# Optimization experiments

Hardware: AMD Instinct MI355X
Metric: run time of the kernel (lower is better)

The kernel has to match this reference:

```python
import jax, jax.numpy as jnp
import numpy as np

jax.config.update("jax_enable_x64", True)

B, S = 256, 256
TINY = float(np.finfo(np.float64).tiny)  # torch.finfo().tiny for double


def _matrix_tree_logZ(scores, mask):
    """scores: [B,S,S] float64, mask: [B,S] bool (col 0 is False).
    Returns sum over batch of log partition function (Matrix-Tree theorem)."""
    lens = mask.sum(-1)  # token counts per sentence (excludes root col)
    mask_r = mask.at[:, 0].set(True)  # index_fill(1, 0, 1)
    pair = mask_r[:, :, None] & mask_r[:, None, :]  # [B,S,S]
    s = jnp.where(pair, scores, -jnp.inf)
    m = jnp.max(s.reshape(s.shape[0], -1), axis=-1)  # [B] per-batch max for stability
    A = jnp.maximum(jnp.exp(s - m[:, None, None]), TINY)  # clamp like torch
    idx = jnp.arange(S)
    D = jnp.zeros_like(A).at[:, idx, idx].set(A.sum(-1))  # degree matrix
    eye = jnp.eye(S, dtype=A.dtype)
    # masked_scatter_: rows with mask_r True take (D - A) rows, else identity
    L = jnp.where(mask_r[:, :, None], D - A, eye)
    logZ = jnp.linalg.slogdet(L[:, 1:, 1:])[1] + m * lens
    return logZ.sum()


def setup_inputs() -> dict:
    key = jax.random.key(0)
    k1, k2 = jax.random.split(key)
    scores = jax.random.normal(k1, (B, S, S), dtype=jnp.float32)
    lens = jax.random.randint(k2, (B,), S // 2, S)  # sentence lengths
    pos = jnp.arange(S)
    # col 0 (pseudo root) False, padding beyond length False
    mask = (pos[None, :] >= 1) & (pos[None, :] < lens[:, None])
    return {"scores": scores, "mask": mask}


def reference(scores, mask):
    # mbr=True path: marginals = d logZ / d scores (computed in double like torch)
    s64 = scores.astype(jnp.float64)
    probs = jax.grad(_matrix_tree_logZ)(s64, mask)
    return probs.astype(jnp.float32)
```

## Files before the change

kernel.cpp:

```cpp
#include <hip/hip_runtime.h>
#include <math.h>


#define S 256
#define BB 256

__device__ __forceinline__ int rowmap(int lr, int kb) {
    int rt = lr >> 6;
    int rb = rt + (rt >= kb ? 1 : 0);
    return rb * 64 + (lr & 63);
}

__global__ __launch_bounds__(256) void k_max(const float* __restrict__ sc,
                                             float* __restrict__ partial) {
    int b = blockIdx.y, rg = blockIdx.x;
    const float4* p4 = (const float4*)(sc + (size_t)b * S * S + rg * 8192);
    int tid = threadIdx.x;
    float4 v[8];
    #pragma unroll
    for (int it = 0; it < 8; ++it) v[it] = p4[tid + 256 * it];
    float m = -1e30f;
    #pragma unroll
    for (int it = 0; it < 8; ++it)
        m = fmaxf(m, fmaxf(fmaxf(v[it].x, v[it].y), fmaxf(v[it].z, v[it].w)));
    for (int off = 32; off > 0; off >>= 1) m = fmaxf(m, __shfl_down(m, off));
    __shared__ float sm[4];
    if ((tid & 63) == 0) sm[tid >> 6] = m;
    __syncthreads();
    if (tid == 0) partial[b * 8 + rg] = fmaxf(fmaxf(sm[0], sm[1]), fmaxf(sm[2], sm[3]));
}

__global__ void k_n(const unsigned char* __restrict__ mk, const float* __restrict__ partial,
                    double* __restrict__ mb, int* __restrict__ nb) {
    int b = blockIdx.x, j = threadIdx.x;
    __shared__ int shc[4];

    const unsigned int* mw = (const unsigned int*)mk;
    unsigned int w0 = mw[0], w1 = mw[1];
    int mode = (w0 != 0u) ? 0 : ((w1 != 0u) ? 1 : 2);

    int c;
    if (mode == 0)      c = (mk[(size_t)b * S + j] != 0);
    else if (mode == 1) c = (((const int*)mk)[(size_t)b * S + j] != 0);
    else                c = (((const long long*)mk)[(size_t)b * S + j] != 0LL);

    int lane = j & 63, wid = j >> 6;
    int cs = c;
    for (int off = 32; off > 0; off >>= 1) cs += __shfl_down(cs, off);
    if (lane == 0) shc[wid] = cs;
    __syncthreads();
    if (j == 0) {
        nb[b] = shc[0] + shc[1] + shc[2] + shc[3];
        float mm = partial[b * 8];
        #pragma unroll
        for (int q = 1; q < 8; ++q) mm = fmaxf(mm, partial[b * 8 + q]);
        mb[b] = (double)mm;
    }
}

__global__ __launch_bounds__(256) void k_build(const float* __restrict__ sc,
                                               const double* __restrict__ mb,
                                               const int* __restrict__ nb,
                                               double* __restrict__ Mg) {
    int b = blockIdx.y;
    int wid = threadIdx.x >> 6, lane = threadIdx.x & 63;
    int p = blockIdx.x * 4 + wid;
    int n = nb[b];
    double m = mb[b];
    __shared__ double se[4][260];
    double* Mrow = Mg + ((size_t)b * S + p) * S;
    bool act = (p < n);
    double ssum = 0.0;
    #pragma unroll
    for (int c4 = 0; c4 < 4; ++c4) {
        int j = lane + 64 * c4;
        double ev = 0.0;
        if (act && j <= n)
            ev = (double)expf((float)((double)sc[((size_t)b * S + (p + 1)) * S + j] - m));
        se[wid][j] = ev;
        ssum += ev;
    }
    for (int off = 32; off > 0; off >>= 1) ssum += __shfl_down(ssum, off);
    ssum = __shfl(ssum, 0);
    __syncthreads();
    #pragma unroll
    for (int c4 = 0; c4 < 4; ++c4) {
        int j = lane + 64 * c4;
        double v;
        if (act && j < n) v = ((j == p) ? ssum : 0.0) - se[wid][j + 1];
        else              v = (j == p) ? 1.0 : 0.0;
        Mrow[j] = v;
    }
}

__global__ __launch_bounds__(512) void k_step(double* __restrict__ Mg, int kb) {
    int b = blockIdx.x;
    double* M = Mg + (size_t)b * S * S;
    int tid = threadIdx.x;
    __shared__ double H[64 * 256];
    __shared__ double SCR[3104];

    int i = tid >> 3, g = tid & 7, c0 = g << 3;
    double c[8];
    {
        const double* src = M + (size_t)(kb * 64 + i) * S + kb * 64 + c0;
        #pragma unroll
        for (int m2 = 0; m2 < 4; ++m2) {
            double2 t = *(const double2*)(src + 2 * m2);
            c[2 * m2] = t.x; c[2 * m2 + 1] = t.y;
        }
    }
    double* rbuf = SCR;
    double* cbuf = SCR + 128;
    if (i == 0) {
        #pragma unroll
        for (int u = 0; u < 8; ++u) rbuf[c0 + u] = c[u];
    }
    if (g == 0) cbuf[i] = c[0];
    for (int k = 0; k < 64; ++k) {
        int par = k & 1;
        __syncthreads();
        double pv = rbuf[par * 64 + k];
        double f  = cbuf[par * 64 + i];
        double rk[8];
        #pragma unroll
        for (int m2 = 0; m2 < 4; ++m2) {
            double2 t = *(const double2*)&rbuf[par * 64 + c0 + 2 * m2];
            rk[2 * m2] = t.x; rk[2 * m2 + 1] = t.y;
        }
        double pivinv = 1.0 / pv;
        int kg = k >> 3, ks = k & 7;
        if (i == k) {
            #pragma unroll
            for (int u = 0; u < 8; ++u)
                c[u] = ((g == kg) && (u == ks)) ? pivinv : c[u] * pivinv;
        } else {
            double gm = f * pivinv;
            #pragma unroll
            for (int u = 0; u < 8; ++u)
                c[u] = ((g == kg) && (u == ks)) ? (-gm) : fma(-gm, rk[u], c[u]);
        }
        int k1 = k + 1;
        if (k1 < 64) {
            if (i == k1) {
                #pragma unroll
                for (int u = 0; u < 8; ++u) rbuf[(par ^ 1) * 64 + c0 + u] = c[u];
            }
            if (g == (k1 >> 3)) cbuf[(par ^ 1) * 64 + i] = c[k1 & 7];
        }
    }
    __syncthreads();

    int tx = tid & 31, ty = tid >> 5;
    double* PT = SCR;
    double* Rc = SCR + 512;
    double2 ga[4][3];
    #pragma unroll
    for (int r = 0; r < 4; ++r)
        #pragma unroll
        for (int q = 0; q < 3; ++q) ga[r][q] = double2{0.0, 0.0};

    for (int cs = 0; cs < 8; ++cs) {
        if (g == cs) {
            #pragma unroll
            for (int u = 0; u < 8; ++u) PT[u * 64 + i] = c[u];
        }
        #pragma unroll
        for (int rep = 0; rep < 3; ++rep) {
            int idx = rep * 512 + tid;
            int sL = idx / 192, jj = idx - sL * 192;
            Rc[sL * 192 + jj] = M[(size_t)(kb * 64 + cs * 8 + sL) * S + rowmap(jj, kb)];
        }
        __syncthreads();
        #pragma unroll
        for (int sL = 0; sL < 8; ++sL) {
            double2 p01 = *(const double2*)&PT[sL * 64 + 4 * ty];
            double2 p23 = *(const double2*)&PT[sL * 64 + 4 * ty + 2];
            double2 r0 = *(const double2*)&Rc[sL * 192 + 2 * tx];
            double2 r1 = *(const double2*)&Rc[sL * 192 + 2 * tx + 64];
            double2 r2 = *(const double2*)&Rc[sL * 192 + 2 * tx + 128];
            ga[0][0].x = fma(p01.x, r0.x, ga[0][0].x); ga[0][0].y = fma(p01.x, r0.y, ga[0][0].y);
            ga[0][1].x = fma(p01.x, r1.x, ga[0][1].x); ga[0][1].y = fma(p01.x, r1.y, ga[0][1].y);
            ga[0][2].x = fma(p01.x, r2.x, ga[0][2].x); ga[0][2].y = fma(p01.x, r2.y, ga[0][2].y);
            ga[1][0].x = fma(p01.y, r0.x, ga[1][0].x); ga[1][0].y = fma(p01.y, r0.y, ga[1][0].y);
            ga[1][1].x = fma(p01.y, r1.x, ga[1][1].x); ga[1][1].y = fma(p01.y, r1.y, ga[1][1].y);
            ga[1][2].x = fma(p01.y, r2.x, ga[1][2].x); ga[1][2].y = fma(p01.y, r2.y, ga[1][2].y);
            ga[2][0].x = fma(p23.x, r0.x, ga[2][0].x); ga[2][0].y = fma(p23.x, r0.y, ga[2][0].y);
            ga[2][1].x = fma(p23.x, r1.x, ga[2][1].x); ga[2][1].y = fma(p23.x, r1.y, ga[2][1].y);
            ga[2][2].x = fma(p23.x, r2.x, ga[2][2].x); ga[2][2].y = fma(p23.x, r2.y, ga[2][2].y);
            ga[3][0].x = fma(p23.y, r0.x, ga[3][0].x); ga[3][0].y = fma(p23.y, r0.y, ga[3][0].y);
            ga[3][1].x = fma(p23.y, r1.x, ga[3][1].x); ga[3][1].y = fma(p23.y, r1.y, ga[3][1].y);
            ga[3][2].x = fma(p23.y, r2.x, ga[3][2].x); ga[3][2].y = fma(p23.y, r2.y, ga[3][2].y);
        }
        __syncthreads();
    }
    #pragma unroll
    for (int r = 0; r < 4; ++r)
        #pragma unroll
        for (int q = 0; q < 3; ++q) {
            int col = rowmap(2 * tx + 64 * q, kb);
            *(double2*)&H[(4 * ty + r) * 256 + col] = ga[r][q];
        }
    #pragma unroll
    for (int u = 0; u < 8; ++u) H[i * 256 + kb * 64 + c0 + u] = c[u];
    __syncthreads();

    #pragma unroll
    for (int rep = 0; rep < 16; ++rep) {
        int idx = rep * 512 + tid;
        int row = idx >> 7, col2 = idx & 127;
        *(double2*)&M[(size_t)(kb * 64 + row) * S + 2 * col2] =
            *(const double2*)&H[row * 256 + 2 * col2];
    }

    double* FT = SCR;
    for (int half = 0; half < 2; ++half) {
        double2 acc[6][4];
        #pragma unroll
        for (int q = 0; q < 6; ++q)
            #pragma unroll
            for (int w = 0; w < 4; ++w) acc[q][w] = double2{0.0, 0.0};

        for (int ck = 0; ck < 4; ++ck) {
            __syncthreads();
            #pragma unroll
            for (int rep = 0; rep < 3; ++rep) {
                int idx = rep * 512 + tid;
                int kk = idx & 15, lr = idx >> 4;
                FT[kk * 194 + lr] =
                    M[(size_t)rowmap(half * 96 + lr, kb) * S + kb * 64 + ck * 16 + kk];
            }
            __syncthreads();
            for (int kk = 0; kk < 16; ++kk) {
                int kr = ck * 16 + kk;
                double2 f01 = *(const double2*)&FT[kk * 194 + 6 * ty];
                double2 f23 = *(const double2*)&FT[kk * 194 + 6 * ty + 2];
                double2 f45 = *(const double2*)&FT[kk * 194 + 6 * ty + 4];
                #pragma unroll
                for (int w = 0; w < 4; ++w) {
                    double2 h = *(const double2*)&H[kr * 256 + 2 * tx + 64 * w];
                    acc[0][w].x = fma(f01.x, h.x, acc[0][w].x); acc[0][w].y = fma(f01.x, h.y, acc[0][w].y);
                    acc[1][w].x = fma(f01.y, h.x, acc[1][w].x); acc[1][w].y = fma(f01.y, h.y, acc[1][w].y);
                    acc[2][w].x = fma(f23.x, h.x, acc[2][w].x); acc[2][w].y = fma(f23.x, h.y, acc[2][w].y);
                    acc[3][w].x = fma(f23.y, h.x, acc[3][w].x); acc[3][w].y = fma(f23.y, h.y, acc[3][w].y);
                    acc[4][w].x = fma(f45.x, h.x, acc[4][w].x); acc[4][w].y = fma(f45.x, h.y, acc[4][w].y);
                    acc[5][w].x = fma(f45.y, h.x, acc[5][w].x); acc[5][w].y = fma(f45.y, h.y, acc[5][w].y);
                }
            }
        }
        #pragma unroll
        for (int q = 0; q < 6; ++q) {
            size_t row = (size_t)rowmap(half * 96 + 6 * ty + q, kb) * S;
            #pragma unroll
            for (int w = 0; w < 4; ++w) {
                int j0 = 2 * tx + 64 * w;
                if (w == kb) {
                    *(double2*)&M[row + j0] = double2{-acc[q][w].x, -acc[q][w].y};
                } else {
                    double2 old = *(const double2*)&M[row + j0];
                    *(double2*)&M[row + j0] = double2{old.x - acc[q][w].x, old.y - acc[q][w].y};
                }
            }
        }
    }
}

__global__ __launch_bounds__(256) void k_xt(const double* __restrict__ Mg,
                                            float* __restrict__ outF,
                                            double* __restrict__ Dg) {
    int b = blockIdx.y, t = blockIdx.x;
    int r = t & 3, c = t >> 2;
    const double* M = Mg + (size_t)b * S * S;
    __shared__ float L[64][65];
    int tid = threadIdx.x;
    int cc = tid & 63;
    #pragma unroll
    for (int rep = 0; rep < 16; ++rep) {
        int rr = rep * 4 + (tid >> 6);
        L[rr][cc] = (float)M[(size_t)(64 * r + rr) * S + 64 * c + cc];
    }
    if (r == c && tid < 64)
        Dg[(size_t)b * S + 64 * r + tid] = M[(size_t)(64 * r + tid) * S + 64 * r + tid];
    __syncthreads();
    int pp = tid & 63;
    #pragma unroll
    for (int rep = 0; rep < 16; ++rep) {
        int qq = rep * 4 + (tid >> 6);
        int orow = 64 * c + qq + 1, ocol = 64 * r + pp + 1;
        if (orow < 256 && ocol < 256)
            outF[((size_t)b * S + orow) * S + ocol] = L[pp][qq];
    }
}

__global__ __launch_bounds__(256) void k_epi2(const float* __restrict__ sc,
                                              const double* __restrict__ Dg,
                                              const double* __restrict__ mb,
                                              const int* __restrict__ nb,
                                              float* __restrict__ out) {
    int b = blockIdx.y;
    int idx4 = blockIdx.x * 256 + threadIdx.x;
    int i = idx4 >> 6;
    int jq = idx4 & 63;
    int n = nb[b];
    float m = (float)mb[b];
    size_t base = ((size_t)b * S + i) * S + 4 * jq;
    float4 xf = *(const float4*)(out + base);
    float4 s4 = *(const float4*)(sc + base);
    double dg = (i >= 1) ? Dg[(size_t)b * S + i - 1] : 0.0;
    float xfa[4] = {xf.x, xf.y, xf.z, xf.w};
    float sa[4]  = {s4.x, s4.y, s4.z, s4.w};
    float ra[4];
    #pragma unroll
    for (int comp = 0; comp < 4; ++comp) {
        int j = 4 * jq + comp;
        float v = 0.0f;
        if (i >= 1 && i <= n && j <= n) {
            double A = (double)expf(sa[comp] - m);
            double sub = (j >= 1) ? (double)xfa[comp] : 0.0;
            v = (float)(A * (dg - sub));
        }
        ra[comp] = v;
    }
    *(float4*)(out + base) = float4{ra[0], ra[1], ra[2], ra[3]};
}

extern "C" void kernel_launch(void* const* d_in, const int* in_sizes, int n_in,
                              void* d_out, int out_size, void* d_ws, size_t ws_size,
                              hipStream_t stream) {
    (void)in_sizes; (void)n_in; (void)out_size; (void)ws_size;
    const float* sc = (const float*)d_in[0];
    const unsigned char* mk = (const unsigned char*)d_in[1];
    double* ws = (double*)d_ws;

    double* M  = ws;
    double* mb = M + (size_t)BB * S * S;
    int*    nb = (int*)(mb + BB);
    double* Dg = mb + 2 * BB;
    float*  partial = (float*)Dg;
    float*  out = (float*)d_out;

    k_max<<<dim3(8, BB), 256, 0, stream>>>(sc, partial);
    k_n<<<BB, 256, 0, stream>>>(mk, partial, mb, nb);
    k_build<<<dim3(64, BB), 256, 0, stream>>>(sc, mb, nb, M);
    for (int kb = 0; kb < 4; ++kb)
        k_step<<<BB, 512, 0, stream>>>(M, kb);
    k_xt<<<dim3(16, BB), 256, 0, stream>>>(M, out, Dg);
    k_epi2<<<dim3(64, BB), 256, 0, stream>>>(sc, Dg, mb, nb, out);
}
```

Measured before the change: 570.7 us.

## Split each block-inversion step across two column-half blocks with double-buffered pivot panel

Each batch's in-place block Gauss-Jordan step now runs as two workgroups, each owning one 128-column half of the matrix. This doubles grid parallelism, and the smaller LDS footprint allows more blocks per CU. The current pivot-column panel is kept in a separate double-buffered F array (placed in the output buffer as scratch). That lets both halves read the unmodified panel without racing on M, and the next panel is written out during the trailing update. The cost is duplicated panel factorization in both blocks, extra global writes for the panel, and reliance on the output buffer being large enough to act as scratch before the final kernels overwrite it.

```diff
diff --git a/kernel.cpp b/kernel.cpp
--- a/kernel.cpp
+++ b/kernel.cpp
@@ -61,7 +61,8 @@
 __global__ __launch_bounds__(256) void k_build(const float* __restrict__ sc,
                                                const double* __restrict__ mb,
                                                const int* __restrict__ nb,
-                                               double* __restrict__ Mg) {
+                                               double* __restrict__ Mg,
+                                               double* __restrict__ Fb) {
     int b = blockIdx.y;
     int wid = threadIdx.x >> 6, lane = threadIdx.x & 63;
     int p = blockIdx.x * 4 + wid;
@@ -90,20 +91,27 @@
         if (act && j < n) v = ((j == p) ? ssum : 0.0) - se[wid][j + 1];
         else              v = (j == p) ? 1.0 : 0.0;
         Mrow[j] = v;
-    }
-}
-
-__global__ __launch_bounds__(512) void k_step(double* __restrict__ Mg, int kb) {
-    int b = blockIdx.x;
+        if (c4 == 0)
+            Fb[((size_t)b * S + p) * 64 + j] = v;
+    }
+}
+
+__global__ __launch_bounds__(512, 4) void k_step2(double* __restrict__ Mg,
+                                                  const double* __restrict__ Fcur,
+                                                  double* __restrict__ Fnext, int kb) {
+    int id = blockIdx.x;
+    int q = id & 1, b = id >> 1;
     double* M = Mg + (size_t)b * S * S;
+    const double* F = Fcur + (size_t)b * (S * 64);
+    double* FN = Fnext + (size_t)b * (S * 64);
     int tid = threadIdx.x;
-    __shared__ double H[64 * 256];
-    __shared__ double SCR[3104];
+    __shared__ double H[64 * 128];
+    __shared__ double SCR[1584];
 
     int i = tid >> 3, g = tid & 7, c0 = g << 3;
     double c[8];
     {
-        const double* src = M + (size_t)(kb * 64 + i) * S + kb * 64 + c0;
+        const double* src = F + (size_t)(kb * 64 + i) * 64 + c0;
         #pragma unroll
         for (int m2 = 0; m2 < 4; ++m2) {
             double2 t = *(const double2*)(src + 2 * m2);
@@ -149,118 +157,129 @@
             if (g == (k1 >> 3)) cbuf[(par ^ 1) * 64 + i] = c[k1 & 7];
         }
     }
-    __syncthreads();
-
-    int tx = tid & 31, ty = tid >> 5;
+
+    int ty = tid >> 5, tx = tid & 31;
     double* PT = SCR;
-    double* Rc = SCR + 512;
-    double2 ga[4][3];
-    #pragma unroll
-    for (int r = 0; r < 4; ++r)
-        #pragma unroll
-        for (int q = 0; q < 3; ++q) ga[r][q] = double2{0.0, 0.0};
-
-    for (int cs = 0; cs < 8; ++cs) {
-        if (g == cs) {
+    double* Rc = SCR + 528;
+    double2 ga[4][2];
+    #pragma unroll
+    for (int r = 0; r < 4; ++r) { ga[r][0] = double2{0.0, 0.0}; ga[r][1] = double2{0.0, 0.0}; }
+
+    for (int cs2 = 0; cs2 < 8; ++cs2) {
+        __syncthreads();
+        if (g == cs2) {
             #pragma unroll
-            for (int u = 0; u < 8; ++u) PT[u * 64 + i] = c[u];
-        }
+            for (int u = 0; u < 8; ++u) PT[u * 66 + i] = c[u];
+        }
+        #pragma unroll
+        for (int rep = 0; rep < 2; ++rep) {
+            int idx = rep * 512 + tid;
+            int kL = idx >> 7, jl = idx & 127;
+            Rc[kL * 132 + jl] = M[(size_t)(kb * 64 + cs2 * 8 + kL) * S + 128 * q + jl];
+        }
+        __syncthreads();
+        #pragma unroll
+        for (int kL = 0; kL < 8; ++kL) {
+            double2 pA = *(const double2*)&PT[kL * 66 + 4 * ty];
+            double2 pB = *(const double2*)&PT[kL * 66 + 4 * ty + 2];
+            double2 r0 = *(const double2*)&Rc[kL * 132 + 2 * tx];
+            double2 r1 = *(const double2*)&Rc[kL * 132 + 2 * tx + 64];
+            ga[0][0].x = fma(pA.x, r0.x, ga[0][0].x); ga[0][0].y = fma(pA.x, r0.y, ga[0][0].y);
+            ga[0][1].x = fma(pA.x, r1.x, ga[0][1].x); ga[0][1].y = fma(pA.x, r1.y, ga[0][1].y);
+            ga[1][0].x = fma(pA.y, r0.x, ga[1][0].x); ga[1][0].y = fma(pA.y, r0.y, ga[1][0].y);
+            ga[1][1].x = fma(pA.y, r1.x, ga[1][1].x); ga[1][1].y = fma(pA.y, r1.y, ga[1][1].y);
+            ga[2][0].x = fma(pB.x, r0.x, ga[2][0].x); ga[2][0].y = fma(pB.x, r0.y, ga[2][0].y);
+            ga[2][1].x = fma(pB.x, r1.x, ga[2][1].x); ga[2][1].y = fma(pB.x, r1.y, ga[2][1].y);
+            ga[3][0].x = fma(pB.y, r0.x, ga[3][0].x); ga[3][0].y = fma(pB.y, r0.y, ga[3][0].y);
+            ga[3][1].x = fma(pB.y, r1.x, ga[3][1].x); ga[3][1].y = fma(pB.y, r1.y, ga[3][1].y);
+        }
+    }
+    #pragma unroll
+    for (int r = 0; r < 4; ++r) {
+        int row = 4 * ty + r;
+        *(double2*)&H[row * 128 + 2 * tx]      = ga[r][0];
+        *(double2*)&H[row * 128 + 64 + 2 * tx] = ga[r][1];
+    }
+    int qp = kb >> 1, po = (kb & 1) << 6;
+    __syncthreads();
+    if (q == qp) {
+        #pragma unroll
+        for (int u = 0; u < 8; ++u) H[i * 128 + po + c0 + u] = c[u];
+    }
+    __syncthreads();
+    #pragma unroll
+    for (int rep = 0; rep < 8; ++rep) {
+        int idx = rep * 512 + tid;
+        int row = idx >> 6, cp = idx & 63;
+        *(double2*)&M[(size_t)(kb * 64 + row) * S + 128 * q + 2 * cp] =
+            *(const double2*)&H[row * 128 + 2 * cp];
+    }
+    int kbn = kb + 1, qn = kbn >> 1, pon = (kbn & 1) << 6;
+    if (kb < 3 && q == qn) {
+        #pragma unroll
+        for (int rep = 0; rep < 4; ++rep) {
+            int idx = rep * 512 + tid;
+            int row = idx >> 5, kp = idx & 31;
+            *(double2*)&FN[(size_t)(kb * 64 + row) * 64 + 2 * kp] =
+                *(const double2*)&H[row * 128 + pon + 2 * kp];
+        }
+    }
+
+    int tz = tid >> 4, txx = tid & 15;
+    double* FT = SCR;
+    double2 acc[6][4];
+    #pragma unroll
+    for (int h = 0; h < 6; ++h)
+        #pragma unroll
+        for (int w = 0; w < 4; ++w) acc[h][w] = double2{0.0, 0.0};
+
+    for (int ck = 0; ck < 8; ++ck) {
+        __syncthreads();
         #pragma unroll
         for (int rep = 0; rep < 3; ++rep) {
             int idx = rep * 512 + tid;
-            int sL = idx / 192, jj = idx - sL * 192;
-            Rc[sL * 192 + jj] = M[(size_t)(kb * 64 + cs * 8 + sL) * S + rowmap(jj, kb)];
-        }
-        __syncthreads();
-        #pragma unroll
-        for (int sL = 0; sL < 8; ++sL) {
-            double2 p01 = *(const double2*)&PT[sL * 64 + 4 * ty];
-            double2 p23 = *(const double2*)&PT[sL * 64 + 4 * ty + 2];
-            double2 r0 = *(const double2*)&Rc[sL * 192 + 2 * tx];
-            double2 r1 = *(const double2*)&Rc[sL * 192 + 2 * tx + 64];
-            double2 r2 = *(const double2*)&Rc[sL * 192 + 2 * tx + 128];
-            ga[0][0].x = fma(p01.x, r0.x, ga[0][0].x); ga[0][0].y = fma(p01.x, r0.y, ga[0][0].y);
-            ga[0][1].x = fma(p01.x, r1.x, ga[0][1].x); ga[0][1].y = fma(p01.x, r1.y, ga[0][1].y);
-            ga[0][2].x = fma(p01.x, r2.x, ga[0][2].x); ga[0][2].y = fma(p01.x, r2.y, ga[0][2].y);
-            ga[1][0].x = fma(p01.y, r0.x, ga[1][0].x); ga[1][0].y = fma(p01.y, r0.y, ga[1][0].y);
-            ga[1][1].x = fma(p01.y, r1.x, ga[1][1].x); ga[1][1].y = fma(p01.y, r1.y, ga[1][1].y);
-            ga[1][2].x = fma(p01.y, r2.x, ga[1][2].x); ga[1][2].y = fma(p01.y, r2.y, ga[1][2].y);
-            ga[2][0].x = fma(p23.x, r0.x, ga[2][0].x); ga[2][0].y = fma(p23.x, r0.y, ga[2][0].y);
-            ga[2][1].x = fma(p23.x, r1.x, ga[2][1].x); ga[2][1].y = fma(p23.x, r1.y, ga[2][1].y);
-            ga[2][2].x = fma(p23.x, r2.x, ga[2][2].x); ga[2][2].y = fma(p23.x, r2.y, ga[2][2].y);
-            ga[3][0].x = fma(p23.y, r0.x, ga[3][0].x); ga[3][0].y = fma(p23.y, r0.y, ga[3][0].y);
-            ga[3][1].x = fma(p23.y, r1.x, ga[3][1].x); ga[3][1].y = fma(p23.y, r1.y, ga[3][1].y);
-            ga[3][2].x = fma(p23.y, r2.x, ga[3][2].x); ga[3][2].y = fma(p23.y, r2.y, ga[3][2].y);
-        }
-        __syncthreads();
-    }
-    #pragma unroll
-    for (int r = 0; r < 4; ++r)
-        #pragma unroll
-        for (int q = 0; q < 3; ++q) {
-            int col = rowmap(2 * tx + 64 * q, kb);
-            *(double2*)&H[(4 * ty + r) * 256 + col] = ga[r][q];
-        }
-    #pragma unroll
-    for (int u = 0; u < 8; ++u) H[i * 256 + kb * 64 + c0 + u] = c[u];
-    __syncthreads();
-
-    #pragma unroll
-    for (int rep = 0; rep < 16; ++rep) {
-        int idx = rep * 512 + tid;
-        int row = idx >> 7, col2 = idx & 127;
-        *(double2*)&M[(size_t)(kb * 64 + row) * S + 2 * col2] =
-            *(const double2*)&H[row * 256 + 2 * col2];
-    }
-
-    double* FT = SCR;
-    for (int half = 0; half < 2; ++half) {
-        double2 acc[6][4];
-        #pragma unroll
-        for (int q = 0; q < 6; ++q)
-            #pragma unroll
-            for (int w = 0; w < 4; ++w) acc[q][w] = double2{0.0, 0.0};
-
-        for (int ck = 0; ck < 4; ++ck) {
-            __syncthreads();
-            #pragma unroll
-            for (int rep = 0; rep < 3; ++rep) {
-                int idx = rep * 512 + tid;
-                int kk = idx & 15, lr = idx >> 4;
-                FT[kk * 194 + lr] =
-                    M[(size_t)rowmap(half * 96 + lr, kb) * S + kb * 64 + ck * 16 + kk];
-            }
-            __syncthreads();
-            for (int kk = 0; kk < 16; ++kk) {
-                int kr = ck * 16 + kk;
-                double2 f01 = *(const double2*)&FT[kk * 194 + 6 * ty];
-                double2 f23 = *(const double2*)&FT[kk * 194 + 6 * ty + 2];
-                double2 f45 = *(const double2*)&FT[kk * 194 + 6 * ty + 4];
-                #pragma unroll
-                for (int w = 0; w < 4; ++w) {
-                    double2 h = *(const double2*)&H[kr * 256 + 2 * tx + 64 * w];
-                    acc[0][w].x = fma(f01.x, h.x, acc[0][w].x); acc[0][w].y = fma(f01.x, h.y, acc[0][w].y);
-                    acc[1][w].x = fma(f01.y, h.x, acc[1][w].x); acc[1][w].y = fma(f01.y, h.y, acc[1][w].y);
-                    acc[2][w].x = fma(f23.x, h.x, acc[2][w].x); acc[2][w].y = fma(f23.x, h.y, acc[2][w].y);
-                    acc[3][w].x = fma(f23.y, h.x, acc[3][w].x); acc[3][w].y = fma(f23.y, h.y, acc[3][w].y);
-                    acc[4][w].x = fma(f45.x, h.x, acc[4][w].x); acc[4][w].y = fma(f45.x, h.y, acc[4][w].y);
-                    acc[5][w].x = fma(f45.y, h.x, acc[5][w].x); acc[5][w].y = fma(f45.y, h.y, acc[5][w].y);
-                }
-            }
-        }
-        #pragma unroll
-        for (int q = 0; q < 6; ++q) {
-            size_t row = (size_t)rowmap(half * 96 + 6 * ty + q, kb) * S;
+            int lr = idx >> 3, kk = idx & 7;
+            FT[kk * 194 + lr] = F[(size_t)rowmap(lr, kb) * 64 + ck * 8 + kk];
+        }
+        __syncthreads();
+        #pragma unroll
+        for (int kk = 0; kk < 8; ++kk) {
+            int kr = ck * 8 + kk;
+            double2 fA = *(const double2*)&FT[kk * 194 + 6 * tz];
+            double2 fB = *(const double2*)&FT[kk * 194 + 6 * tz + 2];
+            double2 fC = *(const double2*)&FT[kk * 194 + 6 * tz + 4];
             #pragma unroll
             for (int w = 0; w < 4; ++w) {
-                int j0 = 2 * tx + 64 * w;
-                if (w == kb) {
-                    *(double2*)&M[row + j0] = double2{-acc[q][w].x, -acc[q][w].y};
-                } else {
-                    double2 old = *(const double2*)&M[row + j0];
-                    *(double2*)&M[row + j0] = double2{old.x - acc[q][w].x, old.y - acc[q][w].y};
-                }
+                double2 h2 = *(const double2*)&H[kr * 128 + 2 * txx + 32 * w];
+                acc[0][w].x = fma(fA.x, h2.x, acc[0][w].x); acc[0][w].y = fma(fA.x, h2.y, acc[0][w].y);
+                acc[1][w].x = fma(fA.y, h2.x, acc[1][w].x); acc[1][w].y = fma(fA.y, h2.y, acc[1][w].y);
+                acc[2][w].x = fma(fB.x, h2.x, acc[2][w].x); acc[2][w].y = fma(fB.x, h2.y, acc[2][w].y);
+                acc[3][w].x = fma(fB.y, h2.x, acc[3][w].x); acc[3][w].y = fma(fB.y, h2.y, acc[3][w].y);
+                acc[4][w].x = fma(fC.x, h2.x, acc[4][w].x); acc[4][w].y = fma(fC.x, h2.y, acc[4][w].y);
+                acc[5][w].x = fma(fC.y, h2.x, acc[5][w].x); acc[5][w].y = fma(fC.y, h2.y, acc[5][w].y);
             }
+        }
+    }
+    bool own_piv  = (q == qp);
+    bool own_next = (kb < 3 && q == qn);
+    #pragma unroll
+    for (int h = 0; h < 6; ++h) {
+        int lr = 6 * tz + h;
+        size_t grow = (size_t)rowmap(lr, kb);
+        size_t base = grow * S + 128 * q;
+        #pragma unroll
+        for (int w = 0; w < 4; ++w) {
+            int j0 = 2 * txx + 32 * w;
+            double2 v;
+            if (own_piv && ((w >> 1) == (po >> 6))) {
+                v = double2{-acc[h][w].x, -acc[h][w].y};
+            } else {
+                double2 old = *(const double2*)&M[base + j0];
+                v = double2{old.x - acc[h][w].x, old.y - acc[h][w].y};
+            }
+            *(double2*)&M[base + j0] = v;
+            if (own_next && ((w >> 1) == (pon >> 6)))
+                *(double2*)&FN[grow * 64 + (j0 - pon)] = v;
         }
     }
 }
@@ -338,12 +357,17 @@
     double* Dg = mb + 2 * BB;
     float*  partial = (float*)Dg;
     float*  out = (float*)d_out;
+    double* Fb0 = (double*)d_out;
+    double* Fb1 = Fb0 + (size_t)BB * S * 64;
 
     k_max<<<dim3(8, BB), 256, 0, stream>>>(sc, partial);
     k_n<<<BB, 256, 0, stream>>>(mk, partial, mb, nb);
-    k_build<<<dim3(64, BB), 256, 0, stream>>>(sc, mb, nb, M);
-    for (int kb = 0; kb < 4; ++kb)
-        k_step<<<BB, 512, 0, stream>>>(M, kb);
+    k_build<<<dim3(64, BB), 256, 0, stream>>>(sc, mb, nb, M, Fb0);
+    for (int kb = 0; kb < 4; ++kb) {
+        const double* Fc = (kb & 1) ? Fb1 : Fb0;
+        double*       Fn = (kb & 1) ? Fb0 : Fb1;
+        k_step2<<<2 * BB, 512, 0, stream>>>(M, Fc, Fn, kb);
+    }
     k_xt<<<dim3(16, BB), 256, 0, stream>>>(M, out, Dg);
     k_epi2<<<dim3(64, BB), 256, 0, stream>>>(sc, Dg, mb, nb, out);
 }
```

After: 673.2 us. 1.18x slower.

## Fuse transpose and epilogue into one kernel with a separate diagonal pass

Applied to the files above, without the earlier changes.

Merges the transpose kernel and the elementwise epilogue into a single kernel that computes the marginals directly from the transposed inverse tile, the scores and the diagonal. A small new kernel extracts the diagonal and writes row 0 and column 0 beforehand. This removes a full write and re-read of the output buffer through global memory. In exchange the scores are read with a transposed-ish per-element pattern and there is one extra small launch.

```diff
diff --git a/kernel.cpp b/kernel.cpp
--- a/kernel.cpp
+++ b/kernel.cpp
@@ -265,13 +265,43 @@
     }
 }
 
-__global__ __launch_bounds__(256) void k_xt(const double* __restrict__ Mg,
-                                            float* __restrict__ outF,
-                                            double* __restrict__ Dg) {
+__global__ __launch_bounds__(256) void k_diag(const double* __restrict__ Mg,
+                                              const float* __restrict__ sc,
+                                              const double* __restrict__ mb,
+                                              const int* __restrict__ nb,
+                                              double* __restrict__ Dg,
+                                              float* __restrict__ out) {
+    int b = blockIdx.x, t = threadIdx.x;
+    const double* M = Mg + (size_t)b * S * S;
+    __shared__ double sd[256];
+    double d = M[(size_t)t * S + t];
+    sd[t] = d;
+    Dg[(size_t)b * S + t] = d;
+    out[(size_t)b * S * S + t] = 0.0f;
+    __syncthreads();
+    int n = nb[b];
+    float m = (float)mb[b];
+    if (t >= 1) {
+        float v = 0.0f;
+        if (t <= n) {
+            double A = (double)expf(sc[((size_t)b * S + t) * S + 0] - m);
+            v = (float)(A * sd[t - 1]);
+        }
+        out[((size_t)b * S + t) * S + 0] = v;
+    }
+}
+
+__global__ __launch_bounds__(256) void k_xtepi(const double* __restrict__ Mg,
+                                               const float* __restrict__ sc,
+                                               const double* __restrict__ mb,
+                                               const int* __restrict__ nb,
+                                               const double* __restrict__ Dg,
+                                               float* __restrict__ out) {
     int b = blockIdx.y, t = blockIdx.x;
     int r = t & 3, c = t >> 2;
     const double* M = Mg + (size_t)b * S * S;
     __shared__ float L[64][65];
+    __shared__ double sdg[64];
     int tid = threadIdx.x;
     int cc = tid & 63;
     #pragma unroll
@@ -279,49 +309,24 @@
         int rr = rep * 4 + (tid >> 6);
         L[rr][cc] = (float)M[(size_t)(64 * r + rr) * S + 64 * c + cc];
     }
-    if (r == c && tid < 64)
-        Dg[(size_t)b * S + 64 * r + tid] = M[(size_t)(64 * r + tid) * S + 64 * r + tid];
-    __syncthreads();
+    if (tid < 64) sdg[tid] = Dg[(size_t)b * S + 64 * c + tid];
+    __syncthreads();
+    int n = nb[b];
+    float m = (float)mb[b];
     int pp = tid & 63;
     #pragma unroll
     for (int rep = 0; rep < 16; ++rep) {
         int qq = rep * 4 + (tid >> 6);
         int orow = 64 * c + qq + 1, ocol = 64 * r + pp + 1;
-        if (orow < 256 && ocol < 256)
-            outF[((size_t)b * S + orow) * S + ocol] = L[pp][qq];
-    }
-}
-
-__global__ __launch_bounds__(256) void k_epi2(const float* __restrict__ sc,
-                                              const double* __restrict__ Dg,
-                                              const double* __restrict__ mb,
-                                              const int* __restrict__ nb,
-                                              float* __restrict__ out) {
-    int b = blockIdx.y;
-    int idx4 = blockIdx.x * 256 + threadIdx.x;
-    int i = idx4 >> 6;
-    int jq = idx4 & 63;
-    int n = nb[b];
-    float m = (float)mb[b];
-    size_t base = ((size_t)b * S + i) * S + 4 * jq;
-    float4 xf = *(const float4*)(out + base);
-    float4 s4 = *(const float4*)(sc + base);
-    double dg = (i >= 1) ? Dg[(size_t)b * S + i - 1] : 0.0;
-    float xfa[4] = {xf.x, xf.y, xf.z, xf.w};
-    float sa[4]  = {s4.x, s4.y, s4.z, s4.w};
-    float ra[4];
-    #pragma unroll
-    for (int comp = 0; comp < 4; ++comp) {
-        int j = 4 * jq + comp;
-        float v = 0.0f;
-        if (i >= 1 && i <= n && j <= n) {
-            double A = (double)expf(sa[comp] - m);
-            double sub = (j >= 1) ? (double)xfa[comp] : 0.0;
-            v = (float)(A * (dg - sub));
-        }
-        ra[comp] = v;
-    }
-    *(float4*)(out + base) = float4{ra[0], ra[1], ra[2], ra[3]};
+        if (orow < 256 && ocol < 256) {
+            float v = 0.0f;
+            if (orow <= n && ocol <= n) {
+                double A = (double)expf(sc[((size_t)b * S + orow) * S + ocol] - m);
+                v = (float)(A * (sdg[qq] - (double)L[pp][qq]));
+            }
+            out[((size_t)b * S + orow) * S + ocol] = v;
+        }
+    }
 }
 
 extern "C" void kernel_launch(void* const* d_in, const int* in_sizes, int n_in,
@@ -344,6 +349,6 @@
     k_build<<<dim3(64, BB), 256, 0, stream>>>(sc, mb, nb, M);
     for (int kb = 0; kb < 4; ++kb)
         k_step<<<BB, 512, 0, stream>>>(M, kb);
-    k_xt<<<dim3(16, BB), 256, 0, stream>>>(M, out, Dg);
-    k_epi2<<<dim3(64, BB), 256, 0, stream>>>(sc, Dg, mb, nb, out);
-}
+    k_diag<<<BB, 256, 0, stream>>>(M, sc, mb, nb, Dg, out);
+    k_xtepi<<<dim3(16, BB), 256, 0, stream>>>(M, sc, mb, nb, Dg, out);
+}
```

After: 549.3 us. 1.04x faster.
